# Kernel optimization log

Measured on AMD Instinct MI355X. Metric: run time of the kernel, lower is better.

## Reference

```python
import jax, jax.numpy as jnp
import numpy as np

HEADS = 4
DIM_HEAD = 64
INNER = HEADS * DIM_HEAD  # 256
MAP_SIZE = (8, 8, 8)
DN = ('NCDHW', 'OIDHW', 'NCDHW')


def _depthwise3d(x, w):
    # x: [B,C,D,H,W], w: [C,1,3,3,3] (torch groups=C layout)
    return jax.lax.conv_general_dilated(
        x, w, window_strides=(1, 1, 1), padding='SAME',
        dimension_numbers=DN, feature_group_count=x.shape[1])


def _dws_conv(x, dw, pw):
    # depthwise 3x3x3 then pointwise 1x1x1 (pw: [out,in])
    y = _depthwise3d(x, dw)
    return jnp.einsum('bcdhw,oc->bodhw', y, pw)


def _split_heads(t):
    # 'b (dim_head heads) d h w -> b heads (d h w) dim_head'
    B, C, D, H, W = t.shape
    t = t.reshape(B, DIM_HEAD, HEADS, D * H * W)
    return t.transpose(0, 2, 3, 1)


def _merge_heads(t, D, H, W):
    # 'b heads n dim_head -> b (dim_head heads) d h w'
    B = t.shape[0]
    return t.transpose(0, 3, 1, 2).reshape(B, DIM_HEAD * HEADS, D, H, W)


def setup_inputs() -> dict:
    key = jax.random.key(0)
    ks = jax.random.split(key, 8)
    B, feat_dim, map_dim, out_dim = 2, 128, 64, 128
    D = H = W = 24
    s = 0.02
    return {
        'feat': jax.random.normal(ks[0], (B, feat_dim, D, H, W), jnp.float32),
        'smap': jax.random.normal(ks[1], (B, map_dim) + MAP_SIZE, jnp.float32),
        'feat_qv_dw': jax.random.normal(ks[2], (feat_dim, 1, 3, 3, 3), jnp.float32) * s,
        'feat_qv_pw': jax.random.normal(ks[3], (2 * INNER, feat_dim), jnp.float32) * s,
        'feat_out_dw': jax.random.normal(ks[4], (INNER, 1, 3, 3, 3), jnp.float32) * s,
        'feat_out_pw': jax.random.normal(ks[5], (out_dim, INNER), jnp.float32) * s,
        'map_qv_w': jax.random.normal(ks[6], (2 * INNER, map_dim), jnp.float32) * s,
        'map_out_w': jax.random.normal(ks[7], (map_dim, INNER), jnp.float32) * s,
    }


def reference(feat, smap, feat_qv_dw, feat_qv_pw, feat_out_dw, feat_out_pw,
              map_qv_w, map_out_w):
    B, C, D, H, W = feat.shape
    scale = DIM_HEAD ** -0.5

    # projections
    fqv = _dws_conv(feat, feat_qv_dw, feat_qv_pw)           # [B, 2*inner, D,H,W]
    feat_q, feat_v = jnp.split(fqv, 2, axis=1)
    mqv = jnp.einsum('bcdhw,oc->bodhw', smap, map_qv_w)     # [B, 2*inner, 8,8,8]
    map_q, map_v = jnp.split(mqv, 2, axis=1)

    feat_q, feat_v = _split_heads(feat_q), _split_heads(feat_v)  # [B,h,N,dh]
    map_q, map_v = _split_heads(map_q), _split_heads(map_v)      # [B,h,M,dh]

    # shared scores, dual-direction softmax
    attn = jnp.einsum('bhid,bhjd->bhij', feat_q, map_q) * scale  # [B,h,N,M]
    feat_map_attn = jax.nn.softmax(attn, axis=-1)
    map_feat_attn = jax.nn.softmax(attn, axis=-2)

    feat_out = jnp.einsum('bhij,bhjd->bhid', feat_map_attn, map_v)   # [B,h,N,dh]
    map_out = jnp.einsum('bhji,bhjd->bhid', map_feat_attn, feat_v)   # [B,h,M,dh]

    feat_out = _merge_heads(feat_out, D, H, W)
    map_out = _merge_heads(map_out, *MAP_SIZE)

    feat_out = _dws_conv(feat_out, feat_out_dw, feat_out_pw)   # [B,out_dim,D,H,W]
    map_out = jnp.einsum('bcdhw,oc->bodhw', map_out, map_out_w)  # [B,map_dim,8,8,8]
    return feat_out, map_out
```

## Files before the change

kernel.cpp:

```cpp
#include <hip/hip_runtime.h>

#define BB 2
#define CH_FEAT 128
#define HEADS 4
#define DH 64
#define INNER 256
#define NPOS 13824
#define MPOS 512
#define DSZ 24
#define JSPLIT 27
#define JCHUNK (NPOS / JSPLIT)

typedef __attribute__((ext_vector_type(8))) short bf16x8;
typedef __attribute__((ext_vector_type(4))) float f32x4;

__device__ inline unsigned short bf16_rn(float x) {
  unsigned u = __builtin_bit_cast(unsigned, x);
  u += 0x7FFF + ((u >> 16) & 1);
  return (unsigned short)(u >> 16);
}
__device__ inline unsigned pk_bf16(float a, float b) {
  return (unsigned)bf16_rn(a) | ((unsigned)bf16_rn(b) << 16);
}
__device__ inline float bf2f(unsigned short u) {
  return __builtin_bit_cast(float, (unsigned)u << 16);
}
__device__ inline float4 ld_bf4(const unsigned short* p) {
  uint2 u = *(const uint2*)p;
  float4 f;
  f.x = __builtin_bit_cast(float, (u.x & 0xFFFFu) << 16);
  f.y = __builtin_bit_cast(float, u.x & 0xFFFF0000u);
  f.z = __builtin_bit_cast(float, (u.y & 0xFFFFu) << 16);
  f.w = __builtin_bit_cast(float, u.y & 0xFFFF0000u);
  return f;
}

#define GL2LDS(g, l)                                                        \
  __builtin_amdgcn_global_load_lds(                                         \
      (const __attribute__((address_space(1))) void*)(g),                   \
      (__attribute__((address_space(3))) void*)(l), 16, 0, 0)

__device__ inline bf16x8 lds_frag(const char* tile, int row, int colb) {
  return *(const bf16x8*)(tile + row * 128 + (colb ^ ((row & 7) << 4)));
}
__device__ inline bf16x8 lds_fragP(const char* tile, int row, int colb, int pitch) {
  return *(const bf16x8*)(tile + row * pitch + (colb ^ ((row & 7) << 4)));
}

__global__ __launch_bounds__(512) void k_map_qv(const float* __restrict__ smap,
                                                const float* __restrict__ w,
                                                unsigned short* __restrict__ mapqb,
                                                unsigned short* __restrict__ mapvTb) {
  int bm = blockIdx.x;
  int b = bm >> 9, m = bm & 511;
  __shared__ float s[64];
  int t = threadIdx.x;
  if (t < 64) s[t] = smap[(size_t)(b * 64 + t) * MPOS + m];
  __syncthreads();
  const float* wr = w + t * 64;
  float acc = 0.f;
#pragma unroll
  for (int c = 0; c < 64; ++c) acc += wr[c] * s[c];
  int qv = t >> 8, c2 = t & 255, head = c2 & 3, dh = c2 >> 2;
  int bh = b * HEADS + head;
  if (qv == 0)
    mapqb[((size_t)bh * MPOS + m) * 64 + dh] = bf16_rn(acc * 0.125f);
  else
    mapvTb[((size_t)bh * 64 + dh) * MPOS + m] = bf16_rn(acc);
}

__global__ __launch_bounds__(256) void k_dwf(const float* __restrict__ in,
                                             const float* __restrict__ w,
                                             unsigned short* __restrict__ out, int C) {
  int tid = blockIdx.x * 256 + threadIdx.x;
  int bc = tid / 1728;
  int s = tid - bc * 1728;
  int c = bc & (C - 1);
  int xs = (s % 3) * 8;
  int row = s / 3;
  int y = row % 24, z = row / 24;
  const float* wr = w + c * 27;
  const float* ip = in + (size_t)bc * NPOS;

  float acc[8];
#pragma unroll
  for (int i = 0; i < 8; ++i) acc[i] = 0.f;

#pragma unroll
  for (int dz = 0; dz < 3; ++dz) {
#pragma unroll
    for (int dy = 0; dy < 3; ++dy) {
      int zz = z + dz - 1, yy = y + dy - 1;
      bool ok = ((unsigned)zz < 24u) && ((unsigned)yy < 24u);
      float w0 = ok ? wr[dz * 9 + dy * 3 + 0] : 0.f;
      float w1 = ok ? wr[dz * 9 + dy * 3 + 1] : 0.f;
      float w2 = ok ? wr[dz * 9 + dy * 3 + 2] : 0.f;
      int zc = min(max(zz, 0), 23), yc = min(max(yy, 0), 23);
      int ro = (zc * 24 + yc) * 24;
      float4 Bv = *(const float4*)(ip + ro + xs);
      float4 Cv = *(const float4*)(ip + ro + xs + 4);
      float xm1 = xs ? *(ip + ro + xs - 1) : 0.f;
      float x8 = (xs < 16) ? *(ip + ro + xs + 8) : 0.f;
      float xv[10] = {xm1, Bv.x, Bv.y, Bv.z, Bv.w, Cv.x, Cv.y, Cv.z, Cv.w, x8};
#pragma unroll
      for (int i = 0; i < 8; ++i)
        acc[i] += w0 * xv[i] + w1 * xv[i + 1] + w2 * xv[i + 2];
    }
  }
  unsigned short* op = out + (size_t)bc * NPOS + row * 24 + xs;
  uint4 pv;
  pv.x = pk_bf16(acc[0], acc[1]);
  pv.y = pk_bf16(acc[2], acc[3]);
  pv.z = pk_bf16(acc[4], acc[5]);
  pv.w = pk_bf16(acc[6], acc[7]);
  *(uint4*)op = pv;
}

__global__ __launch_bounds__(256) void k_dwb(const unsigned short* __restrict__ in,
                                             const float* __restrict__ w,
                                             unsigned short* __restrict__ out, int C) {
  int tid = blockIdx.x * 256 + threadIdx.x;
  int bc = tid / 1728;
  int s = tid - bc * 1728;
  int c = bc & (C - 1), b = bc / C;
  int cm = (c & 63) * 4 + (c >> 6);
  int xs = (s % 3) * 8;
  int row = s / 3;
  int y = row % 24, z = row / 24;
  const float* wr = w + cm * 27;
  const unsigned short* ip = in + (size_t)bc * NPOS;

  float acc[8];
#pragma unroll
  for (int i = 0; i < 8; ++i) acc[i] = 0.f;

#pragma unroll
  for (int dz = 0; dz < 3; ++dz) {
#pragma unroll
    for (int dy = 0; dy < 3; ++dy) {
      int zz = z + dz - 1, yy = y + dy - 1;
      bool ok = ((unsigned)zz < 24u) && ((unsigned)yy < 24u);
      float w0 = ok ? wr[dz * 9 + dy * 3 + 0] : 0.f;
      float w1 = ok ? wr[dz * 9 + dy * 3 + 1] : 0.f;
      float w2 = ok ? wr[dz * 9 + dy * 3 + 2] : 0.f;
      int zc = min(max(zz, 0), 23), yc = min(max(yy, 0), 23);
      int ro = (zc * 24 + yc) * 24;
      float4 Bv = ld_bf4(ip + ro + xs);
      float4 Cv = ld_bf4(ip + ro + xs + 4);
      float xm1 = xs ? bf2f(ip[ro + xs - 1]) : 0.f;
      float x8 = (xs < 16) ? bf2f(ip[ro + xs + 8]) : 0.f;
      float xv[10] = {xm1, Bv.x, Bv.y, Bv.z, Bv.w, Cv.x, Cv.y, Cv.z, Cv.w, x8};
#pragma unroll
      for (int i = 0; i < 8; ++i)
        acc[i] += w0 * xv[i] + w1 * xv[i + 1] + w2 * xv[i + 2];
    }
  }
  unsigned short* op = out + ((size_t)b * C + cm) * NPOS + row * 24 + xs;
  uint4 pv;
  pv.x = pk_bf16(acc[0], acc[1]);
  pv.y = pk_bf16(acc[2], acc[3]);
  pv.z = pk_bf16(acc[4], acc[5]);
  pv.w = pk_bf16(acc[6], acc[7]);
  *(uint4*)op = pv;
}

__global__ __launch_bounds__(256) void k_trb(const unsigned short* __restrict__ in,
                                             unsigned short* __restrict__ outT, int C) {
  __shared__ unsigned sT[64][33];
  int t = threadIdx.x;
  int n0 = blockIdx.x * 64, c0 = blockIdx.y * 64, b = blockIdx.z;
  {
    int r = t >> 2, s8 = (t & 3) * 8;
    const unsigned short* ip = in + ((size_t)b * C + c0 + r) * NPOS + n0 + s8 * 2;
    uint4 a = *(const uint4*)(ip);
    uint4 b2 = *(const uint4*)(ip + 8);
    sT[r][s8 + 0] = a.x; sT[r][s8 + 1] = a.y; sT[r][s8 + 2] = a.z; sT[r][s8 + 3] = a.w;
    sT[r][s8 + 4] = b2.x; sT[r][s8 + 5] = b2.y; sT[r][s8 + 6] = b2.z; sT[r][s8 + 7] = b2.w;
  }
  __syncthreads();
  int nr = t >> 2, cs = (t & 3) * 16;
  int n2 = nr >> 1, nl = (nr & 1) * 16;
  unsigned pkv[8];
#pragma unroll
  for (int i = 0; i < 8; ++i) {
    unsigned lo = (sT[cs + 2 * i][n2] >> nl) & 0xFFFFu;
    unsigned hi = (sT[cs + 2 * i + 1][n2] >> nl) & 0xFFFFu;
    pkv[i] = lo | (hi << 16);
  }
  unsigned short* op = outT + ((size_t)b * NPOS + n0 + nr) * C + c0 + cs;
  *(uint4*)(op) = *(uint4*)&pkv[0];
  *(uint4*)(op + 8) = *(uint4*)&pkv[4];
}

__global__ __launch_bounds__(256) void k_pwqv_m(const unsigned short* __restrict__ dwtT,
                                                const float* __restrict__ pw,
                                                unsigned short* __restrict__ fqb,
                                                unsigned short* __restrict__ fvTb) {
  __shared__ __align__(16) char sAB[49152];
  char* sW = sAB;
  char* sB = sAB + 16384;
  int t = threadIdx.x, wave = t >> 6, lane = t & 63, g = lane >> 4, c = lane & 15;
  int n0 = blockIdx.x * 128, ti = blockIdx.y, b = blockIdx.z;
  int qv = ti >> 2, head = ti & 3, bh = b * 4 + head;

  {
    int r = t >> 2, ks = (t & 3) * 32;
    int co = qv * 256 + r * 4 + head;
    const float* wp = pw + (size_t)co * 128 + ks;
    unsigned pkv[16];
#pragma unroll
    for (int i = 0; i < 8; ++i) {
      float4 v = *(const float4*)(wp + i * 4);
      pkv[2 * i] = pk_bf16(v.x, v.y);
      pkv[2 * i + 1] = pk_bf16(v.z, v.w);
    }
#pragma unroll
    for (int u = 0; u < 4; ++u) {
      int colb = (ks * 2 + u * 16) ^ ((r & 7) << 4);
      *(uint4*)(sW + r * 256 + colb) = *(uint4*)&pkv[u * 4];
    }
  }
  const char* Bg = (const char*)(dwtT + ((size_t)b * NPOS + n0) * 128);
#pragma unroll
  for (int p = 0; p < 8; ++p) {
    int oo = p * 4096 + t * 16;
    int row = oo >> 8, col = (oo & 255) ^ (((oo >> 8) & 7) << 4);
    GL2LDS(Bg + (size_t)row * 256 + col, sB + oo);
  }
  __syncthreads();

  f32x4 acc[4][2];
#pragma unroll
  for (int ct = 0; ct < 4; ++ct)
#pragma unroll
    for (int jf = 0; jf < 2; ++jf) acc[ct][jf] = (f32x4){0.f, 0.f, 0.f, 0.f};
  int nw = wave * 32;
#pragma unroll
  for (int kc = 0; kc < 4; ++kc) {
    bf16x8 bq[2];
#pragma unroll
    for (int jf = 0; jf < 2; ++jf)
      bq[jf] = lds_fragP(sB, nw + jf * 16 + c, kc * 64 + g * 16, 256);
#pragma unroll
    for (int ct = 0; ct < 4; ++ct) {
      bf16x8 a = lds_fragP(sW, ct * 16 + c, kc * 64 + g * 16, 256);
#pragma unroll
      for (int jf = 0; jf < 2; ++jf)
        acc[ct][jf] = __builtin_amdgcn_mfma_f32_16x16x32_bf16(a, bq[jf], acc[ct][jf], 0, 0, 0);
    }
  }
  __syncthreads();

  char* dmp = sB;
#pragma unroll
  for (int ct = 0; ct < 4; ++ct)
#pragma unroll
    for (int jf = 0; jf < 2; ++jf) {
      int n = nw + jf * 16 + c;
      uint2 wv;
      wv.x = pk_bf16(acc[ct][jf][0], acc[ct][jf][1]);
      wv.y = pk_bf16(acc[ct][jf][2], acc[ct][jf][3]);
      *(uint2*)(dmp + n * 144 + (ct * 16 + 4 * g) * 2) = wv;
    }
  __syncthreads();

  if (qv == 0) {
    int nr = t >> 1, seg = t & 1;
    const char* src = dmp + nr * 144 + seg * 64;
    unsigned short* dst = fqb + ((size_t)bh * NPOS + n0 + nr) * 64 + seg * 32;
#pragma unroll
    for (int i = 0; i < 4; ++i)
      *(uint4*)(dst + i * 8) = *(const uint4*)(src + i * 16);
  } else {
#pragma unroll
    for (int it = 0; it < 2; ++it) {
      int idx = it * 256 + t;
      int dh = idx >> 3, nseg = (idx & 7) * 16;
      unsigned pkv[8];
#pragma unroll
      for (int i = 0; i < 8; ++i) {
        unsigned short lo = *(const unsigned short*)(dmp + (nseg + 2 * i) * 144 + dh * 2);
        unsigned short hi = *(const unsigned short*)(dmp + (nseg + 2 * i + 1) * 144 + dh * 2);
        pkv[i] = (unsigned)lo | ((unsigned)hi << 16);
      }
      unsigned short* dst = fvTb + ((size_t)bh * 64 + dh) * NPOS + n0 + nseg;
      *(uint4*)(dst) = *(uint4*)&pkv[0];
      *(uint4*)(dst + 8) = *(uint4*)&pkv[4];
    }
  }
}

__global__ __launch_bounds__(256) void k_pwout_m(const unsigned short* __restrict__ dwoT,
                                                 const float* __restrict__ pw,
                                                 float* __restrict__ out1) {
  __shared__ __align__(16) char sW[32768];
  __shared__ __align__(16) char sB[32768];
  int t = threadIdx.x, wave = t >> 6, lane = t & 63, g = lane >> 4, c = lane & 15;
  int n0 = blockIdx.x * 128, ti = blockIdx.y, b = blockIdx.z;

  {
    int r = t >> 2, ks = (t & 3) * 64;
    const float* wp = pw + (size_t)(ti * 64 + r) * 256 + ks;
    unsigned pkv[32];
#pragma unroll
    for (int i = 0; i < 16; ++i) {
      float4 v = *(const float4*)(wp + i * 4);
      pkv[2 * i] = pk_bf16(v.x, v.y);
      pkv[2 * i + 1] = pk_bf16(v.z, v.w);
    }
#pragma unroll
    for (int u = 0; u < 8; ++u) {
      int colb = (ks * 2 + u * 16) ^ ((r & 7) << 4);
      *(uint4*)(sW + r * 512 + colb) = *(uint4*)&pkv[u * 4];
    }
  }

  f32x4 acc[4][2];
#pragma unroll
  for (int ct = 0; ct < 4; ++ct)
#pragma unroll
    for (int jf = 0; jf < 2; ++jf) acc[ct][jf] = (f32x4){0.f, 0.f, 0.f, 0.f};
  int nw = wave * 32;
  const char* Bg = (const char*)(dwoT + ((size_t)b * NPOS + n0) * 256);

  for (int kh = 0; kh < 2; ++kh) {
#pragma unroll
    for (int p = 0; p < 8; ++p) {
      int oo = p * 4096 + t * 16;
      int row = oo >> 8, col = (oo & 255) ^ (((oo >> 8) & 7) << 4);
      GL2LDS(Bg + (size_t)row * 512 + kh * 256 + col, sB + oo);
    }
    __syncthreads();
#pragma unroll
    for (int kc = 0; kc < 4; ++kc) {
      bf16x8 bq[2];
#pragma unroll
      for (int jf = 0; jf < 2; ++jf)
        bq[jf] = lds_fragP(sB, nw + jf * 16 + c, kc * 64 + g * 16, 256);
#pragma unroll
      for (int ct = 0; ct < 4; ++ct) {
        bf16x8 a = lds_fragP(sW, ct * 16 + c, (kh * 4 + kc) * 64 + g * 16, 512);
#pragma unroll
        for (int jf = 0; jf < 2; ++jf)
          acc[ct][jf] = __builtin_amdgcn_mfma_f32_16x16x32_bf16(a, bq[jf], acc[ct][jf], 0, 0, 0);
      }
    }
    __syncthreads();
  }
#pragma unroll
  for (int ct = 0; ct < 4; ++ct)
#pragma unroll
    for (int jf = 0; jf < 2; ++jf) {
      int n = n0 + nw + jf * 16 + c;
#pragma unroll
      for (int r = 0; r < 4; ++r) {
        int co = ti * 64 + ct * 16 + 4 * g + r;
        out1[((size_t)b * 128 + co) * NPOS + n] = acc[ct][jf][r];
      }
    }
}

__global__ __launch_bounds__(256) void k_attn_row(const unsigned short* __restrict__ fqb,
                                                  const unsigned short* __restrict__ mapqb,
                                                  const unsigned short* __restrict__ mapvTb,
                                                  unsigned short* __restrict__ F) {
  __shared__ __align__(16) char sPool[32768];
  __shared__ __align__(16) unsigned sP[4][2][16][36];
  __shared__ float sL[4][2][16];
  int t = threadIdx.x, wave = t >> 6, lane = t & 63, g = lane >> 4, c = lane & 15;
  int bh = blockIdx.y;
  int j0 = blockIdx.x * 128 + wave * 32;

  const char* Kg = (const char*)(mapqb + (size_t)bh * MPOS * 64);
  const char* Vg = (const char*)(mapvTb + (size_t)bh * 64 * MPOS);

  const unsigned short* fqp = fqb + ((size_t)bh * NPOS + j0 + c) * 64 + 8 * g;
  bf16x8 bq00 = *(const bf16x8*)(fqp);
  bf16x8 bq01 = *(const bf16x8*)(fqp + 32);
  bf16x8 bq10 = *(const bf16x8*)(fqp + 16 * 64);
  bf16x8 bq11 = *(const bf16x8*)(fqp + 16 * 64 + 32);

  f32x4 o[2][4];
#pragma unroll
  for (int jf = 0; jf < 2; ++jf)
#pragma unroll
    for (int dt = 0; dt < 4; ++dt) o[jf][dt] = (f32x4){0.f, 0.f, 0.f, 0.f};
  float ls0 = 0.f, ls1 = 0.f;

#pragma unroll
  for (int p = 0; p < 2; ++p) {
    int oo = p * 4096 + t * 16;
    int row = oo >> 7, col = (oo & 127) ^ (((oo >> 7) & 7) << 4);
    GL2LDS(Kg + (size_t)row * 128 + col, sPool + oo);
    GL2LDS(Vg + (size_t)row * 1024 + col, sPool + 16384 + oo);
  }
  __syncthreads();

  for (int ic = 0; ic < 8; ++ic) {
    const char* Kt = sPool + (ic & 1) * 8192;
    const char* Vt = sPool + 16384 + (ic & 1) * 8192;
    if (ic < 7) {
      int ibase = (ic + 1) * 64;
      int bsel = ((ic + 1) & 1) * 8192;
#pragma unroll
      for (int p = 0; p < 2; ++p) {
        int oo = p * 4096 + t * 16;
        int row = oo >> 7, col = (oo & 127) ^ (((oo >> 7) & 7) << 4);
        GL2LDS(Kg + (size_t)(ibase + row) * 128 + col, sPool + bsel + oo);
        GL2LDS(Vg + (size_t)row * 1024 + ibase * 2 + col, sPool + 16384 + bsel + oo);
      }
    }
#pragma unroll
    for (int ti = 0; ti < 4; ++ti) {
      bf16x8 a0 = lds_frag(Kt, ti * 16 + c, 16 * g);
      bf16x8 a1 = lds_frag(Kt, ti * 16 + c, 64 + 16 * g);
      f32x4 s0 = {0.f, 0.f, 0.f, 0.f}, s1 = {0.f, 0.f, 0.f, 0.f};
      s0 = __builtin_amdgcn_mfma_f32_16x16x32_bf16(a0, bq00, s0, 0, 0, 0);
      s0 = __builtin_amdgcn_mfma_f32_16x16x32_bf16(a1, bq01, s0, 0, 0, 0);
      s1 = __builtin_amdgcn_mfma_f32_16x16x32_bf16(a0, bq10, s1, 0, 0, 0);
      s1 = __builtin_amdgcn_mfma_f32_16x16x32_bf16(a1, bq11, s1, 0, 0, 0);
      float p0 = __expf(s0[0]), p1 = __expf(s0[1]), p2 = __expf(s0[2]), p3 = __expf(s0[3]);
      ls0 += (p0 + p1) + (p2 + p3);
      sP[wave][0][c][ti * 8 + 2 * g] = pk_bf16(p0, p1);
      sP[wave][0][c][ti * 8 + 2 * g + 1] = pk_bf16(p2, p3);
      float q0 = __expf(s1[0]), q1 = __expf(s1[1]), q2 = __expf(s1[2]), q3 = __expf(s1[3]);
      ls1 += (q0 + q1) + (q2 + q3);
      sP[wave][1][c][ti * 8 + 2 * g] = pk_bf16(q0, q1);
      sP[wave][1][c][ti * 8 + 2 * g + 1] = pk_bf16(q2, q3);
    }
#pragma unroll
    for (int ks = 0; ks < 2; ++ks) {
      bf16x8 ap0 = *(const bf16x8*)&sP[wave][0][c][ks * 16 + 4 * g];
      bf16x8 ap1 = *(const bf16x8*)&sP[wave][1][c][ks * 16 + 4 * g];
#pragma unroll
      for (int dt = 0; dt < 4; ++dt) {
        bf16x8 bv = lds_frag(Vt, dt * 16 + c, ks * 64 + 16 * g);
        o[0][dt] = __builtin_amdgcn_mfma_f32_16x16x32_bf16(ap0, bv, o[0][dt], 0, 0, 0);
        o[1][dt] = __builtin_amdgcn_mfma_f32_16x16x32_bf16(ap1, bv, o[1][dt], 0, 0, 0);
      }
    }
    __syncthreads();
  }

  ls0 += __shfl_xor(ls0, 16); ls0 += __shfl_xor(ls0, 32);
  ls1 += __shfl_xor(ls1, 16); ls1 += __shfl_xor(ls1, 32);
  if (g == 0) { sL[wave][0][c] = 1.f / ls0; sL[wave][1][c] = 1.f / ls1; }
#pragma unroll
  for (int jf = 0; jf < 2; ++jf) {
    float rl0 = sL[wave][jf][4 * g + 0], rl1 = sL[wave][jf][4 * g + 1];
    float rl2 = sL[wave][jf][4 * g + 2], rl3 = sL[wave][jf][4 * g + 3];
#pragma unroll
    for (int dt = 0; dt < 4; ++dt) {
      uint2 wv;
      wv.x = pk_bf16(o[jf][dt][0] * rl0, o[jf][dt][1] * rl1);
      wv.y = pk_bf16(o[jf][dt][2] * rl2, o[jf][dt][3] * rl3);
      *(uint2*)(sPool + (dt * 16 + c) * 272 + (wave * 32 + jf * 16 + 4 * g) * 2) = wv;
    }
  }
  __syncthreads();
  {
    int ch = t >> 2, seg = t & 3;
    int b = bh >> 2, head = bh & 3;
    unsigned short* dst = F + ((size_t)b * INNER + head * 64 + ch) * NPOS +
                          blockIdx.x * 128 + seg * 32;
    const char* src = sPool + ch * 272 + seg * 64;
#pragma unroll
    for (int i = 0; i < 4; ++i)
      *(uint4*)(dst + i * 8) = *(const uint4*)(src + i * 16);
  }
}

__global__ __launch_bounds__(256) void k_attn_col(const unsigned short* __restrict__ fqb,
                                                  const unsigned short* __restrict__ fvTb,
                                                  const unsigned short* __restrict__ mapqb,
                                                  float* __restrict__ Gc,
                                                  float* __restrict__ Gl) {
  __shared__ __align__(16) char sQ[2][8192];
  __shared__ __align__(16) char sV[2][8192];
  __shared__ __align__(16) unsigned sP[4][2][16][36];
  int t = threadIdx.x, wave = t >> 6, lane = t & 63, g = lane >> 4, c = lane & 15;
  int bh = blockIdx.x, chunk = blockIdx.z;
  int i0 = blockIdx.y * 128 + wave * 32;
  int jb = chunk * JCHUNK;

  const char* Qg = (const char*)(fqb + (size_t)bh * NPOS * 64);
  const char* Vg = (const char*)(fvTb + (size_t)bh * 64 * NPOS);

  const unsigned short* kp = mapqb + ((size_t)bh * MPOS + i0 + c) * 64 + 8 * g;
  bf16x8 bm00 = *(const bf16x8*)(kp);
  bf16x8 bm01 = *(const bf16x8*)(kp + 32);
  bf16x8 bm10 = *(const bf16x8*)(kp + 16 * 64);
  bf16x8 bm11 = *(const bf16x8*)(kp + 16 * 64 + 32);

  f32x4 o[2][4];
#pragma unroll
  for (int f = 0; f < 2; ++f)
#pragma unroll
    for (int dt = 0; dt < 4; ++dt) o[f][dt] = (f32x4){0.f, 0.f, 0.f, 0.f};
  float lc0 = 0.f, lc1 = 0.f;

#pragma unroll
  for (int p = 0; p < 2; ++p) {
    int oo = p * 4096 + t * 16;
    int row = oo >> 7, col = (oo & 127) ^ (((oo >> 7) & 7) << 4);
    GL2LDS(Qg + (size_t)(jb + row) * 128 + col, sQ[0] + oo);
    GL2LDS(Vg + (size_t)row * (NPOS * 2) + jb * 2 + col, sV[0] + oo);
  }
  __syncthreads();

  for (int jc = 0; jc < JCHUNK / 64; ++jc) {
    const char* Qt = sQ[jc & 1];
    const char* Vt = sV[jc & 1];
    if (jc < JCHUNK / 64 - 1) {
      int jbase = jb + (jc + 1) * 64;
#pragma unroll
      for (int p = 0; p < 2; ++p) {
        int oo = p * 4096 + t * 16;
        int row = oo >> 7, col = (oo & 127) ^ (((oo >> 7) & 7) << 4);
        GL2LDS(Qg + (size_t)(jbase + row) * 128 + col, sQ[(jc + 1) & 1] + oo);
        GL2LDS(Vg + (size_t)row * (NPOS * 2) + jbase * 2 + col, sV[(jc + 1) & 1] + oo);
      }
    }
#pragma unroll
    for (int tj = 0; tj < 4; ++tj) {
      bf16x8 a0 = lds_frag(Qt, tj * 16 + c, 16 * g);
      bf16x8 a1 = lds_frag(Qt, tj * 16 + c, 64 + 16 * g);
      f32x4 s0 = {0.f, 0.f, 0.f, 0.f}, s1 = {0.f, 0.f, 0.f, 0.f};
      s0 = __builtin_amdgcn_mfma_f32_16x16x32_bf16(a0, bm00, s0, 0, 0, 0);
      s0 = __builtin_amdgcn_mfma_f32_16x16x32_bf16(a1, bm01, s0, 0, 0, 0);
      s1 = __builtin_amdgcn_mfma_f32_16x16x32_bf16(a0, bm10, s1, 0, 0, 0);
      s1 = __builtin_amdgcn_mfma_f32_16x16x32_bf16(a1, bm11, s1, 0, 0, 0);
      float p0 = __expf(s0[0]), p1 = __expf(s0[1]), p2 = __expf(s0[2]), p3 = __expf(s0[3]);
      lc0 += (p0 + p1) + (p2 + p3);
      sP[wave][0][c][tj * 8 + 2 * g] = pk_bf16(p0, p1);
      sP[wave][0][c][tj * 8 + 2 * g + 1] = pk_bf16(p2, p3);
      float q0 = __expf(s1[0]), q1 = __expf(s1[1]), q2 = __expf(s1[2]), q3 = __expf(s1[3]);
      lc1 += (q0 + q1) + (q2 + q3);
      sP[wave][1][c][tj * 8 + 2 * g] = pk_bf16(q0, q1);
      sP[wave][1][c][tj * 8 + 2 * g + 1] = pk_bf16(q2, q3);
    }
#pragma unroll
    for (int ks = 0; ks < 2; ++ks) {
      bf16x8 ap0 = *(const bf16x8*)&sP[wave][0][c][ks * 16 + 4 * g];
      bf16x8 ap1 = *(const bf16x8*)&sP[wave][1][c][ks * 16 + 4 * g];
#pragma unroll
      for (int dt = 0; dt < 4; ++dt) {
        bf16x8 bv = lds_frag(Vt, dt * 16 + c, ks * 64 + 16 * g);
        o[0][dt] = __builtin_amdgcn_mfma_f32_16x16x32_bf16(ap0, bv, o[0][dt], 0, 0, 0);
        o[1][dt] = __builtin_amdgcn_mfma_f32_16x16x32_bf16(ap1, bv, o[1][dt], 0, 0, 0);
      }
    }
    __syncthreads();
  }

  lc0 += __shfl_xor(lc0, 16); lc0 += __shfl_xor(lc0, 32);
  lc1 += __shfl_xor(lc1, 16); lc1 += __shfl_xor(lc1, 32);
  int gi = chunk * 8 + bh;
  if (g == 0) {
    Gl[(size_t)gi * MPOS + i0 + c] = lc0;
    Gl[(size_t)gi * MPOS + i0 + 16 + c] = lc1;
  }
  float* gp = Gc + ((size_t)gi * MPOS + i0) * 64;
#pragma unroll
  for (int f = 0; f < 2; ++f)
#pragma unroll
    for (int dt = 0; dt < 4; ++dt)
#pragma unroll
      for (int r = 0; r < 4; ++r)
        gp[(size_t)(f * 16 + 4 * g + r) * 64 + dt * 16 + c] = o[f][dt][r];
}

__global__ __launch_bounds__(256) void k_map_out(const float* __restrict__ Gc,
                                                 const float* __restrict__ Gl,
                                                 const float* __restrict__ mow,
                                                 float* __restrict__ out2) {
  int m = blockIdx.x, b = blockIdx.y, t = threadIdx.x;
  __shared__ float sMA[256];
  __shared__ float sL[4];
  if (t < 4) {
    float l = 0.f;
#pragma unroll 4
    for (int ch = 0; ch < JSPLIT; ++ch) l += Gl[(size_t)(ch * 8 + b * 4 + t) * MPOS + m];
    sL[t] = 1.f / l;
  }
  __syncthreads();
  {
    int head = t & 3, dh = t >> 2;
    int bh = b * 4 + head;
    float a = 0.f;
#pragma unroll 4
    for (int ch = 0; ch < JSPLIT; ++ch)
      a += Gc[((size_t)(ch * 8 + bh) * MPOS + m) * 64 + dh];
    sMA[t] = a * sL[head];
  }
  __syncthreads();
  if (t < 64) {
    const float* wr = mow + t * 256;
    float acc = 0.f;
#pragma unroll 4
    for (int c = 0; c < 256; ++c) acc += wr[c] * sMA[c];
    out2[((size_t)b * 64 + t) * MPOS + m] = acc;
  }
}

extern "C" void kernel_launch(void* const* d_in, const int* in_sizes, int n_in,
                              void* d_out, int out_size, void* d_ws, size_t ws_size,
                              hipStream_t stream) {
  const float* feat = (const float*)d_in[0];
  const float* smap = (const float*)d_in[1];
  const float* fqv_dw = (const float*)d_in[2];
  const float* fqv_pw = (const float*)d_in[3];
  const float* fout_dw = (const float*)d_in[4];
  const float* fout_pw = (const float*)d_in[5];
  const float* mqv_w = (const float*)d_in[6];
  const float* mout_w = (const float*)d_in[7];

  float* out = (float*)d_out;
  float* out1 = out;
  float* out2 = out + (size_t)BB * 128 * NPOS;

  const size_t QV = (size_t)BB * HEADS * NPOS * DH;
  const size_t MQV = (size_t)BB * HEADS * MPOS * DH;
  float* ws = (float*)d_ws;
  unsigned short* F = (unsigned short*)ws;
  unsigned short* fqb = (unsigned short*)(ws + QV);
  unsigned short* fvTb = fqb + QV;
  unsigned short* mapqb = fvTb + QV;
  unsigned short* mapvTb = mapqb + MQV;
  float* Gc = (float*)(mapvTb + MQV);
  float* Gl = Gc + (size_t)JSPLIT * 8 * MPOS * 64;

  unsigned short* dwt = (unsigned short*)out1;
  unsigned short* dwtT = (unsigned short*)Gc;
  unsigned short* dwt2 = fqb;
  unsigned short* dwoT = (unsigned short*)ws;

  k_map_qv<<<dim3(BB * MPOS), dim3(512), 0, stream>>>(smap, mqv_w, mapqb, mapvTb);
  k_dwf<<<dim3(BB * CH_FEAT * 1728 / 256), dim3(256), 0, stream>>>(feat, fqv_dw, dwt, CH_FEAT);
  k_trb<<<dim3(NPOS / 64, CH_FEAT / 64, BB), dim3(256), 0, stream>>>(dwt, dwtT, CH_FEAT);
  k_pwqv_m<<<dim3(NPOS / 128, 8, BB), dim3(256), 0, stream>>>(dwtT, fqv_pw, fqb, fvTb);
  k_attn_row<<<dim3(NPOS / 128, BB * HEADS), dim3(256), 0, stream>>>(fqb, mapqb, mapvTb, F);
  k_attn_col<<<dim3(8, MPOS / 128, JSPLIT), dim3(256), 0, stream>>>(fqb, fvTb, mapqb, Gc, Gl);
  k_map_out<<<dim3(MPOS, BB), dim3(256), 0, stream>>>(Gc, Gl, mout_w, out2);
  k_dwb<<<dim3(BB * INNER * 1728 / 256), dim3(256), 0, stream>>>(F, fout_dw, dwt2, INNER);
  k_trb<<<dim3(NPOS / 64, INNER / 64, BB), dim3(256), 0, stream>>>(dwt2, dwoT, INNER);
  k_pwout_m<<<dim3(NPOS / 128, 2, BB), dim3(256), 0, stream>>>(dwoT, fout_pw, out1);
}
```

Baseline: 205.4 us.

## Fuse channel-major transpose into pointwise GEMM kernels, drop separate transpose passes

Removes the two standalone transpose kernels (k_trb) and has the pointwise-conv MFMA kernels load channel-major tiles straight from global memory into LDS, then transpose them in LDS into the swizzled layout the MFMA fragments expect. This saves two kernel launches and a full write and re-read of the transposed intermediates in global memory. In exchange it adds LDS traffic, extra barriers and a larger LDS footprint per block, which may lower occupancy, and the pwqv kernel re-transposes the same input tile once for each of its 8 y-blocks.

New measurement: 195.9 us. 4.6% less time.

```diff
diff --git a/kernel.cpp b/kernel.cpp
--- a/kernel.cpp
+++ b/kernel.cpp
@@ -164,41 +164,13 @@
   *(uint4*)op = pv;
 }
 
-__global__ __launch_bounds__(256) void k_trb(const unsigned short* __restrict__ in,
-                                             unsigned short* __restrict__ outT, int C) {
-  __shared__ unsigned sT[64][33];
-  int t = threadIdx.x;
-  int n0 = blockIdx.x * 64, c0 = blockIdx.y * 64, b = blockIdx.z;
-  {
-    int r = t >> 2, s8 = (t & 3) * 8;
-    const unsigned short* ip = in + ((size_t)b * C + c0 + r) * NPOS + n0 + s8 * 2;
-    uint4 a = *(const uint4*)(ip);
-    uint4 b2 = *(const uint4*)(ip + 8);
-    sT[r][s8 + 0] = a.x; sT[r][s8 + 1] = a.y; sT[r][s8 + 2] = a.z; sT[r][s8 + 3] = a.w;
-    sT[r][s8 + 4] = b2.x; sT[r][s8 + 5] = b2.y; sT[r][s8 + 6] = b2.z; sT[r][s8 + 7] = b2.w;
-  }
-  __syncthreads();
-  int nr = t >> 2, cs = (t & 3) * 16;
-  int n2 = nr >> 1, nl = (nr & 1) * 16;
-  unsigned pkv[8];
-#pragma unroll
-  for (int i = 0; i < 8; ++i) {
-    unsigned lo = (sT[cs + 2 * i][n2] >> nl) & 0xFFFFu;
-    unsigned hi = (sT[cs + 2 * i + 1][n2] >> nl) & 0xFFFFu;
-    pkv[i] = lo | (hi << 16);
-  }
-  unsigned short* op = outT + ((size_t)b * NPOS + n0 + nr) * C + c0 + cs;
-  *(uint4*)(op) = *(uint4*)&pkv[0];
-  *(uint4*)(op + 8) = *(uint4*)&pkv[4];
-}
-
-__global__ __launch_bounds__(256) void k_pwqv_m(const unsigned short* __restrict__ dwtT,
+__global__ __launch_bounds__(256) void k_pwqv_m(const unsigned short* __restrict__ dwt,
                                                 const float* __restrict__ pw,
                                                 unsigned short* __restrict__ fqb,
                                                 unsigned short* __restrict__ fvTb) {
-  __shared__ __align__(16) char sAB[49152];
-  char* sW = sAB;
-  char* sB = sAB + 16384;
+  __shared__ __align__(16) char sW[16384];
+  __shared__ __align__(16) char sR[32768];
+  __shared__ __align__(16) char sB[32768];
   int t = threadIdx.x, wave = t >> 6, lane = t & 63, g = lane >> 4, c = lane & 15;
   int n0 = blockIdx.x * 128, ti = blockIdx.y, b = blockIdx.z;
   int qv = ti >> 2, head = ti & 3, bh = b * 4 + head;
@@ -220,12 +192,30 @@
       *(uint4*)(sW + r * 256 + colb) = *(uint4*)&pkv[u * 4];
     }
   }
-  const char* Bg = (const char*)(dwtT + ((size_t)b * NPOS + n0) * 128);
+  const char* Bgc = (const char*)(dwt + (size_t)b * CH_FEAT * NPOS);
 #pragma unroll
   for (int p = 0; p < 8; ++p) {
     int oo = p * 4096 + t * 16;
-    int row = oo >> 8, col = (oo & 255) ^ (((oo >> 8) & 7) << 4);
-    GL2LDS(Bg + (size_t)row * 256 + col, sB + oo);
+    int k = oo >> 8, col = oo & 255;
+    GL2LDS(Bgc + (size_t)k * (NPOS * 2) + n0 * 2 + col, sR + oo);
+  }
+  __syncthreads();
+
+  {
+    const unsigned short* R16 = (const unsigned short*)sR;
+#pragma unroll
+    for (int it = 0; it < 8; ++it) {
+      int cid = it * 256 + t;
+      int n = cid & 127, kc16 = (cid >> 7) & 15;
+      unsigned short v[8];
+#pragma unroll
+      for (int j = 0; j < 8; ++j) v[j] = R16[(kc16 * 8 + j) * 128 + n];
+      unsigned u4[4];
+#pragma unroll
+      for (int i = 0; i < 4; ++i)
+        u4[i] = (unsigned)v[2 * i] | ((unsigned)v[2 * i + 1] << 16);
+      *(uint4*)(sB + n * 256 + ((kc16 * 16) ^ ((n & 7) << 4))) = *(uint4*)&u4[0];
+    }
   }
   __syncthreads();
 
@@ -251,7 +241,7 @@
   }
   __syncthreads();
 
-  char* dmp = sB;
+  char* dmp = sR;
 #pragma unroll
   for (int ct = 0; ct < 4; ++ct)
 #pragma unroll
@@ -290,11 +280,12 @@
   }
 }
 
-__global__ __launch_bounds__(256) void k_pwout_m(const unsigned short* __restrict__ dwoT,
+__global__ __launch_bounds__(256) void k_pwout_m(const unsigned short* __restrict__ dwo,
                                                  const float* __restrict__ pw,
                                                  float* __restrict__ out1) {
   __shared__ __align__(16) char sW[32768];
   __shared__ __align__(16) char sB[32768];
+  __shared__ __align__(16) char sR[16384];
   int t = threadIdx.x, wave = t >> 6, lane = t & 63, g = lane >> 4, c = lane & 15;
   int n0 = blockIdx.x * 128, ti = blockIdx.y, b = blockIdx.z;
 
@@ -321,16 +312,36 @@
 #pragma unroll
     for (int jf = 0; jf < 2; ++jf) acc[ct][jf] = (f32x4){0.f, 0.f, 0.f, 0.f};
   int nw = wave * 32;
-  const char* Bg = (const char*)(dwoT + ((size_t)b * NPOS + n0) * 256);
+  const char* Bgc = (const char*)(dwo + (size_t)b * INNER * NPOS);
+  const unsigned short* R16 = (const unsigned short*)sR;
 
   for (int kh = 0; kh < 2; ++kh) {
 #pragma unroll
-    for (int p = 0; p < 8; ++p) {
-      int oo = p * 4096 + t * 16;
-      int row = oo >> 8, col = (oo & 255) ^ (((oo >> 8) & 7) << 4);
-      GL2LDS(Bg + (size_t)row * 512 + kh * 256 + col, sB + oo);
-    }
-    __syncthreads();
+    for (int q = 0; q < 2; ++q) {
+#pragma unroll
+      for (int p = 0; p < 4; ++p) {
+        int oo = p * 4096 + t * 16;
+        int kl = oo >> 8, col = oo & 255;
+        GL2LDS(Bgc + (size_t)(kh * 128 + q * 64 + kl) * (NPOS * 2) + n0 * 2 + col,
+               sR + oo);
+      }
+      __syncthreads();
+#pragma unroll
+      for (int it = 0; it < 4; ++it) {
+        int cid = it * 256 + t;
+        int n = cid & 127, kcl = (cid >> 7) & 7;
+        unsigned short v[8];
+#pragma unroll
+        for (int j = 0; j < 8; ++j) v[j] = R16[(kcl * 8 + j) * 128 + n];
+        unsigned u4[4];
+#pragma unroll
+        for (int i = 0; i < 4; ++i)
+          u4[i] = (unsigned)v[2 * i] | ((unsigned)v[2 * i + 1] << 16);
+        int kc16 = q * 8 + kcl;
+        *(uint4*)(sB + n * 256 + ((kc16 * 16) ^ ((n & 7) << 4))) = *(uint4*)&u4[0];
+      }
+      __syncthreads();
+    }
 #pragma unroll
     for (int kc = 0; kc < 4; ++kc) {
       bf16x8 bq[2];
@@ -631,18 +642,14 @@
   float* Gl = Gc + (size_t)JSPLIT * 8 * MPOS * 64;
 
   unsigned short* dwt = (unsigned short*)out1;
-  unsigned short* dwtT = (unsigned short*)Gc;
   unsigned short* dwt2 = fqb;
-  unsigned short* dwoT = (unsigned short*)ws;
 
   k_map_qv<<<dim3(BB * MPOS), dim3(512), 0, stream>>>(smap, mqv_w, mapqb, mapvTb);
   k_dwf<<<dim3(BB * CH_FEAT * 1728 / 256), dim3(256), 0, stream>>>(feat, fqv_dw, dwt, CH_FEAT);
-  k_trb<<<dim3(NPOS / 64, CH_FEAT / 64, BB), dim3(256), 0, stream>>>(dwt, dwtT, CH_FEAT);
-  k_pwqv_m<<<dim3(NPOS / 128, 8, BB), dim3(256), 0, stream>>>(dwtT, fqv_pw, fqb, fvTb);
+  k_pwqv_m<<<dim3(NPOS / 128, 8, BB), dim3(256), 0, stream>>>(dwt, fqv_pw, fqb, fvTb);
   k_attn_row<<<dim3(NPOS / 128, BB * HEADS), dim3(256), 0, stream>>>(fqb, mapqb, mapvTb, F);
   k_attn_col<<<dim3(8, MPOS / 128, JSPLIT), dim3(256), 0, stream>>>(fqb, fvTb, mapqb, Gc, Gl);
   k_map_out<<<dim3(MPOS, BB), dim3(256), 0, stream>>>(Gc, Gl, mout_w, out2);
   k_dwb<<<dim3(BB * INNER * 1728 / 256), dim3(256), 0, stream>>>(F, fout_dw, dwt2, INNER);
-  k_trb<<<dim3(NPOS / 64, INNER / 64, BB), dim3(256), 0, stream>>>(dwt2, dwoT, INNER);
-  k_pwout_m<<<dim3(NPOS / 128, 2, BB), dim3(256), 0, stream>>>(dwoT, fout_pw, out1);
-}
+  k_pwout_m<<<dim3(NPOS / 128, 2, BB), dim3(256), 0, stream>>>(dwt2, fout_pw, out1);
+}
```
